# Optimization experiments

Hardware: AMD Instinct MI355X
Metric: run time of the kernel (lower is better)

Reference implementation:

```python
import jax, jax.numpy as jnp
import numpy as np
from jax import lax

EPS = 1e-06


def _ema_scan(x, s):
    # x: [B, C, T]; s: [C] smoothing coeff in [0, 1]
    # Recurrence: y_0 = x_0; y_t = s * x_t + (1 - s) * y_{t-1}
    # Expressed as affine pairs (A_t, b_t) with y_t = A_t * y_{t-1} + b_t
    s_b = s[None, :, None]  # [1, C, 1]
    A0 = jnp.zeros_like(x[:, :, :1])
    A_rest = jnp.broadcast_to(1.0 - s_b, x[:, :, 1:].shape)
    A = jnp.concatenate([A0, A_rest], axis=2)
    b = jnp.concatenate([x[:, :, :1], s_b * x[:, :, 1:]], axis=2)

    def combine(c1, c2):
        a1, b1 = c1
        a2, b2 = c2
        return (a1 * a2, a2 * b1 + b2)

    _, ema = lax.associative_scan(combine, (A, b), axis=2)
    return ema


def setup_inputs() -> dict:
    key = jax.random.key(0)
    B, C, T = 32, 128, 16000
    kx, = jax.random.split(key, 1)
    x = jax.random.uniform(kx, (B, C, T), dtype=jnp.float32)
    alpha = jnp.ones((C,), dtype=jnp.float32) * 0.96
    delta = jnp.ones((C,), dtype=jnp.float32) * 2.0
    root = jnp.ones((C,), dtype=jnp.float32) * 2.0
    ema_weights = jnp.ones((C,), dtype=jnp.float32) * 0.04
    return {"x": x, "alpha": alpha, "delta": delta, "root": root, "ema_weights": ema_weights}


def reference(x, alpha, delta, root, ema_weights):
    # sPCEN: per-channel EMA smoother + power-law compression
    s = jnp.clip(ema_weights, 0.0, 1.0)
    ema = _ema_scan(x, s)  # [B, C, T]

    alpha_c = jnp.minimum(alpha, 1.0)[None, :, None]
    root_c = jnp.maximum(root, 1.0)[None, :, None]
    r = 1.0 / root_c
    d = delta[None, :, None]

    out = (x / (EPS + ema) ** alpha_c + d) ** r - d ** r
    return out
```

## Files before the change

kernel.cpp:

```cpp
#include <hip/hip_runtime.h>
#include <math.h>

#define T_LEN    16000
#define T_LEN4   4000
#define THREADS  256
#define CHUNK    17
#define TILE     (THREADS * CHUNK)
#define TILE4    (TILE / 4)
#define NT       4
#define EPS_F    1e-6f

__launch_bounds__(THREADS, 4)
__global__ void pcen_kernel(const float* __restrict__ x,
                            const float* __restrict__ alpha,
                            const float* __restrict__ delta,
                            const float* __restrict__ root,
                            const float* __restrict__ ema_w,
                            float* __restrict__ out, int C) {
    __shared__ __align__(16) float buf[TILE];
    __shared__ float swA[4], swB[4];

    const int row  = blockIdx.x;
    const int c    = row % C;
    const int tid  = threadIdx.x;
    const int lane = tid & 63;
    const int wave = tid >> 6;

    const float s   = fminf(fmaxf(ema_w[c], 0.0f), 1.0f);
    const float q   = 1.0f - s;
    const float a_c = fminf(alpha[c], 1.0f);
    const float r   = 1.0f / fmaxf(root[c], 1.0f);
    const float d   = delta[c];
    const float dr  = powf(d, r);

    const float4* x4 = (const float4*)(x   + (size_t)row * T_LEN);
    float4*       o4 = (float4*)      (out + (size_t)row * T_LEN);
    float4*       b4 = (float4*)buf;

    float e_carry = 0.0f;
    const int lbase = tid * CHUNK;

    for (int t = 0; t < NT; ++t) {
        const int tb4 = t * TILE4;

        #pragma unroll
        for (int k = 0; k < 5; ++k) {
            int i4l = tid + k * THREADS;
            if (i4l < TILE4) {
                int i4 = tb4 + i4l;
                b4[i4l] = (i4 < T_LEN4) ? x4[i4] : make_float4(1.f, 1.f, 1.f, 1.f);
            }
        }
        __syncthreads();

        float a = 1.0f, b = 0.0f;
        #pragma unroll
        for (int j = 0; j < CHUNK; ++j) {
            float xv = buf[lbase + j];
            bool first = (t == 0) & (tid == 0) & (j == 0);
            float xa = first ? 0.0f : q;
            float xb = first ? xv   : s * xv;
            b = fmaf(xa, b, xb);
            a *= xa;
        }

        float la = a, lb = b;
        #pragma unroll
        for (int off = 1; off < 64; off <<= 1) {
            float ua = __shfl_up(la, off);
            float ub = __shfl_up(lb, off);
            if (lane >= off) { lb = fmaf(la, ub, lb); la *= ua; }
        }
        if (lane == 63) { swA[wave] = la; swB[wave] = lb; }
        __syncthreads();

        float pa = 1.0f, pb = 0.0f;
        #pragma unroll
        for (int w = 0; w < 3; ++w) {
            if (w < wave) { pb = fmaf(swA[w], pb, swB[w]); pa *= swA[w]; }
        }
        float ea = __shfl_up(la, 1);
        float eb = __shfl_up(lb, 1);
        float a_ex, b_ex;
        if (lane == 0) { a_ex = pa;      b_ex = pb; }
        else           { a_ex = pa * ea; b_ex = fmaf(ea, pb, eb); }
        float e = fmaf(a_ex, e_carry, b_ex);

        float ta = 1.0f, tb = 0.0f;
        #pragma unroll
        for (int w = 0; w < 4; ++w) { tb = fmaf(swA[w], tb, swB[w]); ta *= swA[w]; }
        e_carry = fmaf(ta, e_carry, tb);

        #pragma unroll
        for (int j = 0; j < CHUNK; ++j) {
            float xv = buf[lbase + j];
            bool first = (t == 0) & (tid == 0) & (j == 0);
            e = first ? xv : fmaf(q, e, s * xv);
            float lge = log2f(EPS_F + e);
            float lgx = log2f(xv);
            float v   = exp2f(fmaf(-a_c, lge, lgx));
            float o   = exp2f(r * log2f(v + d)) - dr;
            buf[lbase + j] = o;
        }
        __syncthreads();

        #pragma unroll
        for (int k = 0; k < 5; ++k) {
            int i4l = tid + k * THREADS;
            if (i4l < TILE4) {
                int i4 = tb4 + i4l;
                if (i4 < T_LEN4) o4[i4] = b4[i4l];
            }
        }
        __syncthreads();
    }
}

extern "C" void kernel_launch(void* const* d_in, const int* in_sizes, int n_in,
                              void* d_out, int out_size, void* d_ws, size_t ws_size,
                              hipStream_t stream) {
    const float* x     = (const float*)d_in[0];
    const float* alpha = (const float*)d_in[1];
    const float* delta = (const float*)d_in[2];
    const float* root  = (const float*)d_in[3];
    const float* ema_w = (const float*)d_in[4];
    float* out = (float*)d_out;

    const int C    = in_sizes[1];
    const int rows = in_sizes[0] / T_LEN;

    pcen_kernel<<<rows, THREADS, 0, stream>>>(x, alpha, delta, root, ema_w, out, C);
}
```

Before: 452.8 us.

## Double-buffer tiles with register prefetch and specialize sqrt power path

```diff
diff --git a/kernel.cpp b/kernel.cpp
--- a/kernel.cpp
+++ b/kernel.cpp
@@ -17,7 +17,7 @@
                             const float* __restrict__ root,
                             const float* __restrict__ ema_w,
                             float* __restrict__ out, int C) {
-    __shared__ __align__(16) float buf[TILE];
+    __shared__ __align__(16) float buf[2][TILE];
     __shared__ float swA[4], swB[4];
 
     const int row  = blockIdx.x;
@@ -32,39 +32,52 @@
     const float r   = 1.0f / fmaxf(root[c], 1.0f);
     const float d   = delta[c];
     const float dr  = powf(d, r);
+    const float q17 = powf(q, (float)CHUNK);
+    const bool  sqrt_path = (r == 0.5f);
 
     const float4* x4 = (const float4*)(x   + (size_t)row * T_LEN);
     float4*       o4 = (float4*)      (out + (size_t)row * T_LEN);
-    float4*       b4 = (float4*)buf;
 
+    const int lbase = tid * CHUNK;
     float e_carry = 0.0f;
-    const int lbase = tid * CHUNK;
+
+    float4 g0, g1, g2, g3, g4 = make_float4(1.f, 1.f, 1.f, 1.f);
+
+    auto load_tile = [&](int t) {
+        const int b = t * TILE4;
+        g0 = (b + tid        < T_LEN4) ? x4[b + tid       ] : make_float4(1.f,1.f,1.f,1.f);
+        g1 = (b + tid +  256 < T_LEN4) ? x4[b + tid +  256] : make_float4(1.f,1.f,1.f,1.f);
+        g2 = (b + tid +  512 < T_LEN4) ? x4[b + tid +  512] : make_float4(1.f,1.f,1.f,1.f);
+        g3 = (b + tid +  768 < T_LEN4) ? x4[b + tid +  768] : make_float4(1.f,1.f,1.f,1.f);
+        if (tid < TILE4 - 1024)
+            g4 = (b + tid + 1024 < T_LEN4) ? x4[b + tid + 1024] : make_float4(1.f,1.f,1.f,1.f);
+    };
+
+    load_tile(0);
 
     for (int t = 0; t < NT; ++t) {
-        const int tb4 = t * TILE4;
+        float*  cb  = &buf[t & 1][0];
+        float4* cb4 = (float4*)cb;
 
-        #pragma unroll
-        for (int k = 0; k < 5; ++k) {
-            int i4l = tid + k * THREADS;
-            if (i4l < TILE4) {
-                int i4 = tb4 + i4l;
-                b4[i4l] = (i4 < T_LEN4) ? x4[i4] : make_float4(1.f, 1.f, 1.f, 1.f);
-            }
-        }
+        cb4[tid]       = g0;
+        cb4[tid + 256] = g1;
+        cb4[tid + 512] = g2;
+        cb4[tid + 768] = g3;
+        if (tid < TILE4 - 1024) cb4[tid + 1024] = g4;
         __syncthreads();
 
-        float a = 1.0f, b = 0.0f;
+        if (t + 1 < NT) load_tile(t + 1);
+
+        float xv[CHUNK];
         #pragma unroll
-        for (int j = 0; j < CHUNK; ++j) {
-            float xv = buf[lbase + j];
-            bool first = (t == 0) & (tid == 0) & (j == 0);
-            float xa = first ? 0.0f : q;
-            float xb = first ? xv   : s * xv;
-            b = fmaf(xa, b, xb);
-            a *= xa;
-        }
+        for (int j = 0; j < CHUNK; ++j) xv[j] = cb[lbase + j];
 
-        float la = a, lb = b;
+        const bool ft = (t == 0) && (tid == 0);
+        float la = ft ? 0.0f   : q17;
+        float lb = ft ? xv[0]  : s * xv[0];
+        #pragma unroll
+        for (int j = 1; j < CHUNK; ++j) lb = fmaf(q, lb, s * xv[j]);
+
         #pragma unroll
         for (int off = 1; off < 64; off <<= 1) {
             float ua = __shfl_up(la, off);
@@ -76,9 +89,9 @@
 
         float pa = 1.0f, pb = 0.0f;
         #pragma unroll
-        for (int w = 0; w < 3; ++w) {
+        for (int w = 0; w < 3; ++w)
             if (w < wave) { pb = fmaf(swA[w], pb, swB[w]); pa *= swA[w]; }
-        }
+
         float ea = __shfl_up(la, 1);
         float eb = __shfl_up(lb, 1);
         float a_ex, b_ex;
@@ -91,28 +104,38 @@
         for (int w = 0; w < 4; ++w) { tb = fmaf(swA[w], tb, swB[w]); ta *= swA[w]; }
         e_carry = fmaf(ta, e_carry, tb);
 
-        #pragma unroll
-        for (int j = 0; j < CHUNK; ++j) {
-            float xv = buf[lbase + j];
-            bool first = (t == 0) & (tid == 0) & (j == 0);
-            e = first ? xv : fmaf(q, e, s * xv);
-            float lge = log2f(EPS_F + e);
-            float lgx = log2f(xv);
-            float v   = exp2f(fmaf(-a_c, lge, lgx));
-            float o   = exp2f(r * log2f(v + d)) - dr;
-            buf[lbase + j] = o;
+        if (t * TILE + lbase < T_LEN) {
+            if (sqrt_path) {
+                #pragma unroll
+                for (int j = 0; j < CHUNK; ++j) {
+                    float xvj = xv[j];
+                    e = (ft && j == 0) ? xvj : fmaf(q, e, s * xvj);
+                    float lge = log2f(EPS_F + e);
+                    float v   = xvj * exp2f(-a_c * lge);
+                    cb[lbase + j] = sqrtf(v + d) - dr;
+                }
+            } else {
+                #pragma unroll
+                for (int j = 0; j < CHUNK; ++j) {
+                    float xvj = xv[j];
+                    e = (ft && j == 0) ? xvj : fmaf(q, e, s * xvj);
+                    float lge = log2f(EPS_F + e);
+                    float v   = xvj * exp2f(-a_c * lge);
+                    cb[lbase + j] = exp2f(r * log2f(v + d)) - dr;
+                }
+            }
         }
         __syncthreads();
 
-        #pragma unroll
-        for (int k = 0; k < 5; ++k) {
-            int i4l = tid + k * THREADS;
-            if (i4l < TILE4) {
-                int i4 = tb4 + i4l;
-                if (i4 < T_LEN4) o4[i4] = b4[i4l];
-            }
+        {
+            const int b = t * TILE4;
+            if (b + tid        < T_LEN4) o4[b + tid       ] = cb4[tid];
+            if (b + tid +  256 < T_LEN4) o4[b + tid +  256] = cb4[tid + 256];
+            if (b + tid +  512 < T_LEN4) o4[b + tid +  512] = cb4[tid + 512];
+            if (b + tid +  768 < T_LEN4) o4[b + tid +  768] = cb4[tid + 768];
+            if (tid < TILE4 - 1024 && b + tid + 1024 < T_LEN4)
+                o4[b + tid + 1024] = cb4[tid + 1024];
         }
-        __syncthreads();
     }
 }
 
```

Result: no change. 447.6 us (-1.2%).
